# Kernel tuning notes

Hardware: AMD Instinct MI355X
Metric: run time of the kernel (lower is better)

Reference implementation:

```python
import jax, jax.numpy as jnp
import numpy as np

NEG_BIG = -1e16  # matches the torch module's mask multiplier (fits in fp32)


def setup_inputs() -> dict:
    key = jax.random.key(0)
    k1, k2, k3, k4 = jax.random.split(key, 4)
    B, S, T, D, O = 8, 2048, 2048, 1024, 1024
    src = jax.random.normal(k1, (B, S, D), dtype=jnp.float32)
    tgt = jax.random.normal(k2, (B, T, D), dtype=jnp.float32)
    mask = jax.random.randint(k3, (T, B, S), 0, 2, dtype=jnp.int32)
    W = jax.random.normal(k4, (O, 2 * D), dtype=jnp.float32) * (1.0 / np.sqrt(2 * D))
    b = jnp.zeros((O,), dtype=jnp.float32)
    return {"src": src, "tgt": tgt, "mask": mask, "W": W, "b": b}


def reference(src, tgt, mask, W, b):
    # scores: [B, T, S] = tgt @ src^T
    weight = jnp.einsum('btd,bsd->bts', tgt, src)
    # mask [T,B,S] -> [B,T,S], additive large-negative where mask==1
    weight = weight + mask.transpose(1, 0, 2).astype(weight.dtype) * NEG_BIG
    # NOTE: original softmax is over dim=1 (the tgt axis), faithful here
    weight = jax.nn.softmax(weight, axis=1)
    weight_sum = jnp.einsum('bts,bsd->btd', weight, src)  # [B,T,D]
    cat = jnp.concatenate([weight_sum, tgt], axis=2)      # [B,T,2D]
    output = cat @ W.T + b                                 # [B,T,O]
    return output, weight
```

## Files before the change

### kernel.cpp

```cpp
#include <hip/hip_runtime.h>

#define Bb 8
#define Ss 2048
#define Tt 2048
#define Dd 1024
#define Oo 1024
#define NEG_BIG -1.0e16f

typedef unsigned short u16;
typedef unsigned int u32;
typedef __attribute__((ext_vector_type(4))) float f32x4;
typedef __attribute__((ext_vector_type(8))) _Float16 f16x8;
typedef __attribute__((ext_vector_type(8))) u16 u16x8;
typedef __attribute__((ext_vector_type(4))) u16 u16x4;

__device__ __forceinline__ u16 f2h(float x) {
  return __builtin_bit_cast(u16, (_Float16)x);
}

__device__ __forceinline__ void gload_lds16(const void* g, void* l) {
  __builtin_amdgcn_global_load_lds(
      (__attribute__((address_space(1))) void*)const_cast<void*>(g),
      (__attribute__((address_space(3))) void*)l, 16, 0, 0);
}

__device__ __forceinline__ f16x8 ldfrag(const u16* p) {
  return __builtin_bit_cast(f16x8, *(const u16x8*)p);
}

__global__ __launch_bounds__(256) void cvt_f16(const float* __restrict__ in,
                                               u16* __restrict__ out16) {
  const size_t i = ((size_t)blockIdx.x * 256 + threadIdx.x) * 4;
  float4 v = *(const float4*)(in + i);
  u16x4 h = {f2h(v.x), f2h(v.y), f2h(v.z), f2h(v.w)};
  *(u16x4*)(out16 + i) = h;
}

__global__ __launch_bounds__(256) void pack_mask(const int* __restrict__ mask,
                                                 u32* __restrict__ bits) {
  const size_t widx = (size_t)blockIdx.x * 256 + threadIdx.x;
  const int sw = (int)(widx & (Ss / 32 - 1));
  const int t = (int)((widx >> 6) & (Tt - 1));
  const int b = (int)(widx >> 17);
  const int* p = mask + ((size_t)t * Bb + b) * Ss + sw * 32;
  u32 w = 0;
#pragma unroll
  for (int q = 0; q < 8; ++q) {
    int4 v = *(const int4*)(p + q * 4);
    w |= (u32)((v.x != 0) ? 1u : 0u) << (q * 4 + 0);
    w |= (u32)((v.y != 0) ? 1u : 0u) << (q * 4 + 1);
    w |= (u32)((v.z != 0) ? 1u : 0u) << (q * 4 + 2);
    w |= (u32)((v.w != 0) ? 1u : 0u) << (q * 4 + 3);
  }
  bits[widx] = w;
}

__global__ __launch_bounds__(256) void prep_src(const float* __restrict__ src,
                                                u16* __restrict__ src16,
                                                u16* __restrict__ srcT) {
  __shared__ u16 tile[64][72];
  const int b = blockIdx.z;
  const int d0 = blockIdx.x * 64;
  const int s0 = blockIdx.y * 64;
  const int tid = threadIdx.x;
  const int sl = tid >> 4;
  const int dl = (tid & 15) * 4;
#pragma unroll
  for (int p = 0; p < 4; ++p) {
    const int srow = s0 + sl + p * 16;
    float4 v = *(const float4*)(src + ((size_t)b * Ss + srow) * Dd + d0 + dl);
    u16 h0 = f2h(v.x), h1 = f2h(v.y), h2 = f2h(v.z), h3 = f2h(v.w);
    *(u16x4*)(src16 + ((size_t)b * Ss + srow) * Dd + d0 + dl) = (u16x4){h0, h1, h2, h3};
    tile[dl + 0][sl + p * 16] = h0;
    tile[dl + 1][sl + p * 16] = h1;
    tile[dl + 2][sl + p * 16] = h2;
    tile[dl + 3][sl + p * 16] = h3;
  }
  __syncthreads();
  const int dl2 = tid >> 4;
  const int sl2 = (tid & 15) * 4;
#pragma unroll
  for (int p = 0; p < 4; ++p) {
    const int drow = d0 + dl2 + p * 16;
    u16x4 vv = {tile[dl2 + p * 16][sl2], tile[dl2 + p * 16][sl2 + 1],
                tile[dl2 + p * 16][sl2 + 2], tile[dl2 + p * 16][sl2 + 3]};
    *(u16x4*)(srcT + ((size_t)b * Dd + drow) * Ss + s0 + sl2) = vv;
  }
}

template <int MODE>
__global__ __launch_bounds__(512) void gemm256(
    const u16* __restrict__ A, size_t ldA, size_t sA,
    const u16* __restrict__ A2,
    const u16* __restrict__ Bm, size_t ldB, size_t sB,
    int NT,
    float* __restrict__ outF, u16* __restrict__ outH,
    const float* __restrict__ bias) {
  __shared__ __align__(16) u16 sh[66560];
  const int b = blockIdx.z;
  const int tn = blockIdx.x, tm = blockIdx.y;
  const int tid = threadIdx.x;
  const int w = tid >> 6, l = tid & 63;
  const int wr = w >> 2, wc = w & 3;

  const int sr0 = w * 16 + (l >> 3);
  const int scb = (((l & 7) ^ (l >> 3)) << 4);
  const int fc0 = (((l >> 4) * 16) ^ ((l & 7) << 4)) >> 1;
  const int fc1 = ((64 + (l >> 4) * 16) ^ ((l & 7) << 4)) >> 1;

  auto STAGE = [&](int isB, int ds, int hh, int ts) {
    int dst = (isB ? 32768 : 0) + ds * 16384 + hh * 8192 + w * 1024;
    if (ts >= NT) { ts = NT - 1; dst = 65536; }
    const u16* srcBase;
    size_t ld;
    int rowBase;
    int kbyte = ts * 128;
    if (isB) {
      srcBase = Bm + (size_t)b * sB;
      ld = ldB;
      rowBase = tn * 256 + hh * 128;
    } else {
      if constexpr (MODE == 2) {
        srcBase = (ts < 16 ? A : A2) + (size_t)b * sA;
        kbyte = (ts & 15) * 128;
      } else {
        srcBase = A + (size_t)b * sA;
      }
      ld = ldA;
      rowBase = tm * 256 + hh * 128;
    }
    const char* s0 = (const char*)srcBase + (size_t)(rowBase + sr0) * (ld * 2) + kbyte + scb;
    const char* s1 = (const char*)srcBase + (size_t)(rowBase + sr0 + 8) * (ld * 2) + kbyte + scb;
    gload_lds16(s0, &sh[dst]);
    gload_lds16(s1, &sh[dst + 512]);
  };

  f32x4 acc[8][4];
#pragma unroll
  for (int m = 0; m < 8; ++m)
#pragma unroll
    for (int n = 0; n < 4; ++n) acc[m][n] = (f32x4){0.f, 0.f, 0.f, 0.f};
  f16x8 bf[4][2], af[2][2];

  STAGE(1, 0, 0, 0);
  STAGE(1, 0, 1, 0);
  STAGE(0, 0, 0, 0);
  STAGE(0, 0, 1, 0);
  STAGE(1, 1, 0, 1);
  STAGE(1, 1, 1, 1);
  asm volatile("s_waitcnt vmcnt(4)" ::: "memory");
  asm volatile("s_barrier" ::: "memory");

  const int NITER = NT >> 1;
  for (int it = 0; it < NITER; ++it) {
#pragma unroll
    for (int p = 0; p < 8; ++p) {
      const int q = p & 3, d = (p >> 2) & 1;
      if (q == 0) {
#pragma unroll
        for (int ni = 0; ni < 4; ++ni) {
          const int rb = wc * 64 + ni * 16 + (l & 15);
          bf[ni][0] = ldfrag(&sh[32768 + d * 16384 + rb * 64 + fc0]);
          bf[ni][1] = ldfrag(&sh[32768 + d * 16384 + rb * 64 + fc1]);
        }
      }
#pragma unroll
      for (int mi = 0; mi < 2; ++mi) {
        const int ra = wr * 128 + q * 32 + mi * 16 + (l & 15);
        af[mi][0] = ldfrag(&sh[d * 16384 + ra * 64 + fc0]);
        af[mi][1] = ldfrag(&sh[d * 16384 + ra * 64 + fc1]);
      }
      {
        const int j = 8 * it + p + 6;
        const int ts = j >> 2, sub = j & 3;
        STAGE(sub < 2, ts & 1, sub & 1, ts);
      }
      if (q == 3) asm volatile("s_waitcnt vmcnt(4)" ::: "memory");
      asm volatile("s_barrier" ::: "memory");
      __builtin_amdgcn_s_setprio(1);
#pragma unroll
      for (int mi = 0; mi < 2; ++mi)
#pragma unroll
        for (int ni = 0; ni < 4; ++ni) {
          acc[2 * q + mi][ni] = __builtin_amdgcn_mfma_f32_16x16x32_f16(
              af[mi][0], bf[ni][0], acc[2 * q + mi][ni], 0, 0, 0);
          acc[2 * q + mi][ni] = __builtin_amdgcn_mfma_f32_16x16x32_f16(
              af[mi][1], bf[ni][1], acc[2 * q + mi][ni], 0, 0, 0);
        }
      __builtin_amdgcn_s_setprio(0);
      asm volatile("s_barrier" ::: "memory");
    }
  }

  const int fr = l & 15, fq = l >> 4;
  const int r0 = tm * 256 + wr * 128;
  const int c0 = tn * 256 + wc * 64;
#pragma unroll
  for (int m = 0; m < 8; ++m) {
#pragma unroll
    for (int n = 0; n < 4; ++n) {
#pragma unroll
      for (int j = 0; j < 4; ++j) {
        const int r = r0 + m * 16 + fq * 4 + j;
        const int c = c0 + n * 16 + fr;
        float v = acc[m][n][j];
        if constexpr (MODE == 0) {
          outF[((size_t)b * Tt + r) * Ss + c] = v;
        } else if constexpr (MODE == 1) {
          outH[((size_t)b * Tt + r) * Dd + c] = f2h(v);
        } else {
          outF[((size_t)b * Tt + r) * Oo + c] = v + bias[c];
        }
      }
    }
  }
}

__global__ __launch_bounds__(512) void colstats(const float* __restrict__ sc,
                                                const u32* __restrict__ bits,
                                                float* __restrict__ mcol,
                                                float* __restrict__ rlcol) {
  const int b = blockIdx.y;
  const int c = threadIdx.x & 63;
  const int seg = threadIdx.x >> 6;
  const int s = blockIdx.x * 64 + c;
  const int sh5 = s & 31;
  float m = -3.0e38f, lsum = 0.0f;
#pragma unroll 4
  for (int i = 0; i < 256; ++i) {
    const size_t idx = ((size_t)b * Tt + seg * 256 + i) * Ss + s;
    float v = sc[idx];
    const u32 wbits = bits[idx >> 5];
    v += (float)((wbits >> sh5) & 1u) * NEG_BIG;
    float mn = fmaxf(m, v);
    lsum = lsum * __expf(m - mn) + __expf(v - mn);
    m = mn;
  }
  __shared__ float sm[8][64], sl[8][64];
  sm[seg][c] = m;
  sl[seg][c] = lsum;
  __syncthreads();
  if (seg == 0) {
    float M = sm[0][c];
#pragma unroll
    for (int k = 1; k < 8; ++k) M = fmaxf(M, sm[k][c]);
    float L = 0.0f;
#pragma unroll
    for (int k = 0; k < 8; ++k) L += sl[k][c] * __expf(sm[k][c] - M);
    mcol[(size_t)b * Ss + s] = M;
    rlcol[(size_t)b * Ss + s] = 1.0f / L;
  }
}

__global__ __launch_bounds__(256) void normalize(float* __restrict__ sc,
                                                 const u32* __restrict__ bits,
                                                 const float* __restrict__ mcol,
                                                 const float* __restrict__ rlcol,
                                                 u16* __restrict__ w16) {
  const size_t i = ((size_t)blockIdx.x * 256 + threadIdx.x) * 4;
  const int s = (int)(i & (Ss - 1));
  const int b = (int)(i >> 22);
  const u32 wbits = bits[i >> 5];
  const int sh5 = s & 31;
  float4 v = *(const float4*)(sc + i);
  float4 m4 = *(const float4*)(mcol + (size_t)b * Ss + s);
  float4 r4 = *(const float4*)(rlcol + (size_t)b * Ss + s);
  float v0 = v.x + (float)((wbits >> (sh5 + 0)) & 1u) * NEG_BIG;
  float v1 = v.y + (float)((wbits >> (sh5 + 1)) & 1u) * NEG_BIG;
  float v2 = v.z + (float)((wbits >> (sh5 + 2)) & 1u) * NEG_BIG;
  float v3 = v.w + (float)((wbits >> (sh5 + 3)) & 1u) * NEG_BIG;
  float w0 = __expf(v0 - m4.x) * r4.x;
  float w1 = __expf(v1 - m4.y) * r4.y;
  float w2 = __expf(v2 - m4.z) * r4.z;
  float w3 = __expf(v3 - m4.w) * r4.w;
  *(float4*)(sc + i) = make_float4(w0, w1, w2, w3);
  *(u16x4*)(w16 + i) = (u16x4){f2h(w0), f2h(w1), f2h(w2), f2h(w3)};
}

extern "C" void kernel_launch(void* const* d_in, const int* in_sizes, int n_in,
                              void* d_out, int out_size, void* d_ws, size_t ws_size,
                              hipStream_t stream) {
  const float* src = (const float*)d_in[0];
  const float* tgt = (const float*)d_in[1];
  const int* mask = (const int*)d_in[2];
  const float* W = (const float*)d_in[3];
  const float* bias = (const float*)d_in[4];
  float* out = (float*)d_out;
  float* scores = out + (size_t)Bb * Tt * Oo;

  u16* tgt16 = (u16*)d_ws;
  u16* src16 = tgt16 + (size_t)Bb * Tt * Dd;
  u16* srcT = src16 + (size_t)Bb * Ss * Dd;
  u16* wsum16 = srcT + (size_t)Bb * Dd * Ss;
  u16* w16 = wsum16 + (size_t)Bb * Tt * Dd;
  u16* W16 = w16 + (size_t)Bb * Tt * Ss;
  float* mcol = (float*)(W16 + (size_t)Oo * 2 * Dd);
  float* rlcol = mcol + (size_t)Bb * Ss;
  u32* bits = (u32*)wsum16;

  pack_mask<<<(Bb * Tt * (Ss / 32)) / 256, 256, 0, stream>>>(mask, bits);
  cvt_f16<<<(Bb * Tt * Dd) / 1024, 256, 0, stream>>>(tgt, tgt16);
  cvt_f16<<<(Oo * 2 * Dd) / 1024, 256, 0, stream>>>(W, W16);
  prep_src<<<dim3(Dd / 64, Ss / 64, Bb), 256, 0, stream>>>(src, src16, srcT);

  gemm256<0><<<dim3(Ss / 256, Tt / 256, Bb), 512, 0, stream>>>(
      tgt16, (size_t)Dd, (size_t)Tt * Dd, nullptr,
      src16, (size_t)Dd, (size_t)Ss * Dd, Dd / 64,
      scores, nullptr, nullptr);

  colstats<<<dim3(Ss / 64, Bb), 512, 0, stream>>>(scores, bits, mcol, rlcol);
  normalize<<<(size_t)(Bb * Tt) * Ss / 1024, 256, 0, stream>>>(scores, bits, mcol, rlcol, w16);

  gemm256<1><<<dim3(Dd / 256, Tt / 256, Bb), 512, 0, stream>>>(
      w16, (size_t)Ss, (size_t)Tt * Ss, nullptr,
      srcT, (size_t)Ss, (size_t)Dd * Ss, Ss / 64,
      nullptr, wsum16, nullptr);

  gemm256<2><<<dim3(Oo / 256, Tt / 256, Bb), 512, 0, stream>>>(
      wsum16, (size_t)Dd, (size_t)Tt * Dd, tgt16,
      W16, (size_t)2 * Dd, (size_t)0, 2 * Dd / 64,
      out, nullptr, bias);
}
```

Before: 668.1 us.

## Fuse masking and column softmax stats into score GEMM epilogue via atomic CAS

The score GEMM epilogue now applies the mask and computes per-column online max/sum. These are reduced across lanes with shuffles and merged into a global packed (max,sum) array through a 64-bit atomicCAS loop. This removes the separate colstats kernel, which re-read the full fp32 score matrix, and drops the mask lookup from normalize. The GEMM inner loop also switches to inline-asm ds_read_b128 with an explicit lgkmcnt wait and sched barriers. The CAS loop caps retries at 64, which could silently drop updates under heavy contention, and it adds atomic traffic plus an init kernel.

```diff
diff --git a/kernel.cpp b/kernel.cpp
--- a/kernel.cpp
+++ b/kernel.cpp
@@ -9,6 +9,7 @@
 
 typedef unsigned short u16;
 typedef unsigned int u32;
+typedef unsigned long long u64;
 typedef __attribute__((ext_vector_type(4))) float f32x4;
 typedef __attribute__((ext_vector_type(8))) _Float16 f16x8;
 typedef __attribute__((ext_vector_type(8))) u16 u16x8;
@@ -24,8 +25,39 @@
       (__attribute__((address_space(3))) void*)l, 16, 0, 0);
 }
 
-__device__ __forceinline__ f16x8 ldfrag(const u16* p) {
-  return __builtin_bit_cast(f16x8, *(const u16x8*)p);
+__device__ __forceinline__ f16x8 ds_read_b128a(const u16* p) {
+  f16x8 r;
+  const __attribute__((address_space(3))) u16* lp =
+      (const __attribute__((address_space(3))) u16*)p;
+  asm volatile("ds_read_b128 %0, %1" : "=v"(r) : "v"(lp));
+  return r;
+}
+
+union F2U {
+  float2 f;
+  u64 u;
+};
+
+__device__ __forceinline__ void ml_cas(u64* addr, float m, float l) {
+  F2U cur;
+  cur.u = *((volatile u64*)addr);
+  for (int it = 0; it < 64; ++it) {
+    float M = fmaxf(cur.f.x, m);
+    float L = cur.f.y * __expf(cur.f.x - M) + l * __expf(m - M);
+    F2U nxt;
+    nxt.f.x = M;
+    nxt.f.y = L;
+    u64 prev = atomicCAS(addr, cur.u, nxt.u);
+    if (prev == cur.u) break;
+    cur.u = prev;
+  }
+}
+
+__global__ __launch_bounds__(256) void init_ml(u64* __restrict__ ml) {
+  F2U v;
+  v.f.x = -3.0e38f;
+  v.f.y = 0.0f;
+  ml[(size_t)blockIdx.x * 256 + threadIdx.x] = v.u;
 }
 
 __global__ __launch_bounds__(256) void cvt_f16(const float* __restrict__ in,
@@ -95,7 +127,8 @@
     const u16* __restrict__ Bm, size_t ldB, size_t sB,
     int NT,
     float* __restrict__ outF, u16* __restrict__ outH,
-    const float* __restrict__ bias) {
+    const float* __restrict__ bias,
+    const u32* __restrict__ bits, u64* __restrict__ ml) {
   __shared__ __align__(16) u16 sh[66560];
   const int b = blockIdx.z;
   const int tn = blockIdx.x, tm = blockIdx.y;
@@ -160,15 +193,15 @@
 #pragma unroll
         for (int ni = 0; ni < 4; ++ni) {
           const int rb = wc * 64 + ni * 16 + (l & 15);
-          bf[ni][0] = ldfrag(&sh[32768 + d * 16384 + rb * 64 + fc0]);
-          bf[ni][1] = ldfrag(&sh[32768 + d * 16384 + rb * 64 + fc1]);
+          bf[ni][0] = ds_read_b128a(&sh[32768 + d * 16384 + rb * 64 + fc0]);
+          bf[ni][1] = ds_read_b128a(&sh[32768 + d * 16384 + rb * 64 + fc1]);
         }
       }
 #pragma unroll
       for (int mi = 0; mi < 2; ++mi) {
         const int ra = wr * 128 + q * 32 + mi * 16 + (l & 15);
-        af[mi][0] = ldfrag(&sh[d * 16384 + ra * 64 + fc0]);
-        af[mi][1] = ldfrag(&sh[d * 16384 + ra * 64 + fc1]);
+        af[mi][0] = ds_read_b128a(&sh[d * 16384 + ra * 64 + fc0]);
+        af[mi][1] = ds_read_b128a(&sh[d * 16384 + ra * 64 + fc1]);
       }
       {
         const int j = 8 * it + p + 6;
@@ -177,6 +210,8 @@
       }
       if (q == 3) asm volatile("s_waitcnt vmcnt(4)" ::: "memory");
       asm volatile("s_barrier" ::: "memory");
+      asm volatile("s_waitcnt lgkmcnt(0)" ::: "memory");
+      __builtin_amdgcn_sched_barrier(0);
       __builtin_amdgcn_s_setprio(1);
 #pragma unroll
       for (int mi = 0; mi < 2; ++mi)
@@ -187,6 +222,7 @@
           acc[2 * q + mi][ni] = __builtin_amdgcn_mfma_f32_16x16x32_f16(
               af[mi][1], bf[ni][1], acc[2 * q + mi][ni], 0, 0, 0);
         }
+      __builtin_amdgcn_sched_barrier(0);
       __builtin_amdgcn_s_setprio(0);
       asm volatile("s_barrier" ::: "memory");
     }
@@ -195,84 +231,80 @@
   const int fr = l & 15, fq = l >> 4;
   const int r0 = tm * 256 + wr * 128;
   const int c0 = tn * 256 + wc * 64;
-#pragma unroll
-  for (int m = 0; m < 8; ++m) {
+  if constexpr (MODE == 0) {
+    float cm[4], cl[4];
+#pragma unroll
+    for (int n = 0; n < 4; ++n) { cm[n] = -3.0e38f; cl[n] = 0.0f; }
+#pragma unroll
+    for (int m = 0; m < 8; ++m) {
+#pragma unroll
+      for (int j = 0; j < 4; ++j) {
+        const int gr = r0 + m * 16 + fq * 4 + j;
+        const u32* bw = bits + ((size_t)b * Tt + gr) * (Ss / 32) + (c0 >> 5);
+        const u32 w0 = bw[0], w1 = bw[1];
+        float* orow = outF + ((size_t)b * Tt + gr) * Ss + c0 + fr;
+#pragma unroll
+        for (int n = 0; n < 4; ++n) {
+          const u32 ww = (n & 2) ? w1 : w0;
+          float v = acc[m][n][j] + (float)((ww >> ((n & 1) * 16 + fr)) & 1u) * NEG_BIG;
+          orow[n * 16] = v;
+          float M = fmaxf(cm[n], v);
+          cl[n] = cl[n] * __expf(cm[n] - M) + __expf(v - M);
+          cm[n] = M;
+        }
+      }
+    }
 #pragma unroll
     for (int n = 0; n < 4; ++n) {
 #pragma unroll
-      for (int j = 0; j < 4; ++j) {
-        const int r = r0 + m * 16 + fq * 4 + j;
-        const int c = c0 + n * 16 + fr;
-        float v = acc[m][n][j];
-        if constexpr (MODE == 0) {
-          outF[((size_t)b * Tt + r) * Ss + c] = v;
-        } else if constexpr (MODE == 1) {
-          outH[((size_t)b * Tt + r) * Dd + c] = f2h(v);
-        } else {
-          outF[((size_t)b * Tt + r) * Oo + c] = v + bias[c];
+      for (int off = 16; off < 64; off <<= 1) {
+        float om = __shfl_xor(cm[n], off);
+        float ol = __shfl_xor(cl[n], off);
+        float M = fmaxf(cm[n], om);
+        cl[n] = cl[n] * __expf(cm[n] - M) + ol * __expf(om - M);
+        cm[n] = M;
+      }
+    }
+    if (l < 16) {
+#pragma unroll
+      for (int n = 0; n < 4; ++n)
+        ml_cas(ml + (size_t)b * Ss + c0 + n * 16 + l, cm[n], cl[n]);
+    }
+  } else {
+#pragma unroll
+    for (int m = 0; m < 8; ++m) {
+#pragma unroll
+      for (int n = 0; n < 4; ++n) {
+#pragma unroll
+        for (int j = 0; j < 4; ++j) {
+          const int r = r0 + m * 16 + fq * 4 + j;
+          const int c = c0 + n * 16 + fr;
+          float v = acc[m][n][j];
+          if constexpr (MODE == 1) {
+            outH[((size_t)b * Tt + r) * Dd + c] = f2h(v);
+          } else {
+            outF[((size_t)b * Tt + r) * Oo + c] = v + bias[c];
+          }
         }
       }
     }
   }
 }
 
-__global__ __launch_bounds__(512) void colstats(const float* __restrict__ sc,
-                                                const u32* __restrict__ bits,
-                                                float* __restrict__ mcol,
-                                                float* __restrict__ rlcol) {
-  const int b = blockIdx.y;
-  const int c = threadIdx.x & 63;
-  const int seg = threadIdx.x >> 6;
-  const int s = blockIdx.x * 64 + c;
-  const int sh5 = s & 31;
-  float m = -3.0e38f, lsum = 0.0f;
-#pragma unroll 4
-  for (int i = 0; i < 256; ++i) {
-    const size_t idx = ((size_t)b * Tt + seg * 256 + i) * Ss + s;
-    float v = sc[idx];
-    const u32 wbits = bits[idx >> 5];
-    v += (float)((wbits >> sh5) & 1u) * NEG_BIG;
-    float mn = fmaxf(m, v);
-    lsum = lsum * __expf(m - mn) + __expf(v - mn);
-    m = mn;
-  }
-  __shared__ float sm[8][64], sl[8][64];
-  sm[seg][c] = m;
-  sl[seg][c] = lsum;
-  __syncthreads();
-  if (seg == 0) {
-    float M = sm[0][c];
-#pragma unroll
-    for (int k = 1; k < 8; ++k) M = fmaxf(M, sm[k][c]);
-    float L = 0.0f;
-#pragma unroll
-    for (int k = 0; k < 8; ++k) L += sl[k][c] * __expf(sm[k][c] - M);
-    mcol[(size_t)b * Ss + s] = M;
-    rlcol[(size_t)b * Ss + s] = 1.0f / L;
-  }
-}
-
 __global__ __launch_bounds__(256) void normalize(float* __restrict__ sc,
-                                                 const u32* __restrict__ bits,
-                                                 const float* __restrict__ mcol,
-                                                 const float* __restrict__ rlcol,
+                                                 const u64* __restrict__ ml,
                                                  u16* __restrict__ w16) {
   const size_t i = ((size_t)blockIdx.x * 256 + threadIdx.x) * 4;
   const int s = (int)(i & (Ss - 1));
   const int b = (int)(i >> 22);
-  const u32 wbits = bits[i >> 5];
-  const int sh5 = s & 31;
   float4 v = *(const float4*)(sc + i);
-  float4 m4 = *(const float4*)(mcol + (size_t)b * Ss + s);
-  float4 r4 = *(const float4*)(rlcol + (size_t)b * Ss + s);
-  float v0 = v.x + (float)((wbits >> (sh5 + 0)) & 1u) * NEG_BIG;
-  float v1 = v.y + (float)((wbits >> (sh5 + 1)) & 1u) * NEG_BIG;
-  float v2 = v.z + (float)((wbits >> (sh5 + 2)) & 1u) * NEG_BIG;
-  float v3 = v.w + (float)((wbits >> (sh5 + 3)) & 1u) * NEG_BIG;
-  float w0 = __expf(v0 - m4.x) * r4.x;
-  float w1 = __expf(v1 - m4.y) * r4.y;
-  float w2 = __expf(v2 - m4.z) * r4.z;
-  float w3 = __expf(v3 - m4.w) * r4.w;
+  const float* mlp = (const float*)(ml + (size_t)b * Ss + s);
+  float4 a = *(const float4*)(mlp);
+  float4 c = *(const float4*)(mlp + 4);
+  float w0 = __expf(v.x - a.x) / a.y;
+  float w1 = __expf(v.y - a.z) / a.w;
+  float w2 = __expf(v.z - c.x) / c.y;
+  float w3 = __expf(v.w - c.z) / c.w;
   *(float4*)(sc + i) = make_float4(w0, w1, w2, w3);
   *(u16x4*)(w16 + i) = (u16x4){f2h(w0), f2h(w1), f2h(w2), f2h(w3)};
 }
@@ -294,10 +326,10 @@
   u16* wsum16 = srcT + (size_t)Bb * Dd * Ss;
   u16* w16 = wsum16 + (size_t)Bb * Tt * Dd;
   u16* W16 = w16 + (size_t)Bb * Tt * Ss;
-  float* mcol = (float*)(W16 + (size_t)Oo * 2 * Dd);
-  float* rlcol = mcol + (size_t)Bb * Ss;
+  u64* ml = (u64*)(W16 + (size_t)Oo * 2 * Dd);
   u32* bits = (u32*)wsum16;
 
+  init_ml<<<(Bb * Ss) / 256, 256, 0, stream>>>(ml);
   pack_mask<<<(Bb * Tt * (Ss / 32)) / 256, 256, 0, stream>>>(mask, bits);
   cvt_f16<<<(Bb * Tt * Dd) / 1024, 256, 0, stream>>>(tgt, tgt16);
   cvt_f16<<<(Oo * 2 * Dd) / 1024, 256, 0, stream>>>(W, W16);
@@ -306,18 +338,17 @@
   gemm256<0><<<dim3(Ss / 256, Tt / 256, Bb), 512, 0, stream>>>(
       tgt16, (size_t)Dd, (size_t)Tt * Dd, nullptr,
       src16, (size_t)Dd, (size_t)Ss * Dd, Dd / 64,
-      scores, nullptr, nullptr);
-
-  colstats<<<dim3(Ss / 64, Bb), 512, 0, stream>>>(scores, bits, mcol, rlcol);
-  normalize<<<(size_t)(Bb * Tt) * Ss / 1024, 256, 0, stream>>>(scores, bits, mcol, rlcol, w16);
+      scores, nullptr, nullptr, bits, ml);
+
+  normalize<<<(size_t)(Bb * Tt) * Ss / 1024, 256, 0, stream>>>(scores, ml, w16);
 
   gemm256<1><<<dim3(Dd / 256, Tt / 256, Bb), 512, 0, stream>>>(
       w16, (size_t)Ss, (size_t)Tt * Ss, nullptr,
       srcT, (size_t)Ss, (size_t)Dd * Ss, Ss / 64,
-      nullptr, wsum16, nullptr);
+      nullptr, wsum16, nullptr, nullptr, nullptr);
 
   gemm256<2><<<dim3(Oo / 256, Tt / 256, Bb), 512, 0, stream>>>(
       wsum16, (size_t)Dd, (size_t)Tt * Dd, tgt16,
       W16, (size_t)2 * Dd, (size_t)0, 2 * Dd / 64,
-      out, nullptr, bias);
-}
+      out, nullptr, bias, nullptr, nullptr);
+}
```

Measured after the change: 664.3 us. No clear change (-0.6%).
